# Kernel optimization log

Measured on AMD Instinct MI355X. Metric: run time of the kernel, lower is better.

Reference implementation:

```python
import jax, jax.numpy as jnp
import numpy as np

DIM_H = 128
N_EXPERTS = 4
N_GRAPHS = 256
EPS = 1e-5


def setup_inputs() -> dict:
    key = jax.random.key(0)
    ks = jax.random.split(key, 16)
    N, E, D = 100000, 1600000, DIM_H
    x = jax.random.normal(ks[0], (N, D), dtype=jnp.float32)
    edge_index = jax.random.randint(ks[1], (2, E), 0, N, dtype=jnp.int64)
    batch = jnp.sort(jax.random.randint(ks[2], (N,), 0, N_GRAPHS, dtype=jnp.int64))
    s = 0.05
    gin = 2 * D + 4  # router input: mean | max | 4 graph stats
    params = dict(
        temperature=jnp.ones((1,), jnp.float32) * 2.0,
        rw1=jax.random.normal(ks[3], (gin, D), jnp.float32) * s,
        rb1=jnp.zeros((D,), jnp.float32),
        rw2=jax.random.normal(ks[4], (D, D // 2), jnp.float32) * s,
        rb2=jnp.zeros((D // 2,), jnp.float32),
        rw3=jax.random.normal(ks[5], (D // 2, N_EXPERTS), jnp.float32) * s,
        rb3=jnp.zeros((N_EXPERTS,), jnp.float32),
        expert_w=jax.random.normal(ks[6], (N_EXPERTS, D, D), jnp.float32) * s,
        expert_b=jnp.zeros((N_EXPERTS, D), jnp.float32),
        bn1_g=jnp.ones((D,), jnp.float32),
        bn1_b=jnp.zeros((D,), jnp.float32),
        ff_w1=jax.random.normal(ks[7], (D, 2 * D), jnp.float32) * s,
        ff_b1=jnp.zeros((2 * D,), jnp.float32),
        ff_w2=jax.random.normal(ks[8], (2 * D, D), jnp.float32) * s,
        ff_b2=jnp.zeros((D,), jnp.float32),
        bn2_g=jnp.ones((D,), jnp.float32),
        bn2_b=jnp.zeros((D,), jnp.float32),
    )
    return dict(x=x, edge_index=edge_index, batch=batch, **params)


def _gcn_agg(x, src, dst, n):
    deg = jnp.zeros((n,), x.dtype).at[dst].add(1.0) + 1.0
    dinv = jax.lax.rsqrt(deg)
    coef = dinv[src] * dinv[dst]                        # [E]
    agg = jax.ops.segment_sum(x[src] * coef[:, None], dst, num_segments=n)
    return agg + x * (1.0 / deg)[:, None]               # self-loop term (coef = 1/deg)


def _batchnorm(h, g, b):
    mu = jnp.mean(h, axis=0)
    var = jnp.var(h, axis=0)
    return (h - mu) * jax.lax.rsqrt(var + EPS) * g + b


def reference(x, edge_index, batch, temperature, rw1, rb1, rw2, rb2, rw3, rb3,
              expert_w, expert_b, bn1_g, bn1_b, ff_w1, ff_b1, ff_w2, ff_b2,
              bn2_g, bn2_b):
    n = x.shape[0]
    src, dst = edge_index[0], edge_index[1]
    B = N_GRAPHS

    # ---- graph embeddings: [mean_pool | max_pool | 4 stats] -> [B, 2D+4] ----
    cnt = jnp.maximum(jax.ops.segment_sum(jnp.ones((n,), x.dtype), batch, num_segments=B), 1.0)
    gmean = jax.ops.segment_sum(x, batch, num_segments=B) / cnt[:, None]
    gmax = jax.ops.segment_max(x, batch, num_segments=B)
    node_deg = jnp.zeros((n,), x.dtype).at[dst].add(1.0)
    mean_deg = jax.ops.segment_sum(node_deg, batch, num_segments=B) / cnt
    max_deg = jax.ops.segment_max(node_deg, batch, num_segments=B)
    stats = jnp.stack([cnt, mean_deg, max_deg, jnp.log(cnt)], axis=-1)  # [B,4]
    ge = jnp.concatenate([gmean, gmax, stats], axis=-1)

    # ---- router: MLP + temperature softmax -> [B, E] ----
    h = jax.nn.relu(ge @ rw1 + rb1)
    h = jax.nn.relu(h @ rw2 + rb2)
    scores = h @ rw3 + rb3
    gates = jax.nn.softmax(scores / temperature, axis=-1)   # [B, n_experts]

    # ---- experts: GCNConv_i(x). Aggregation is linear so do it once. ----
    agg = _gcn_agg(x, src, dst, n)                          # [N, D]
    expert_out = jnp.einsum('nd,edo->neo', agg, expert_w) + expert_b[None]  # [N,E,D]

    # ---- softmax-gated combine with per-graph gates ----
    kv = jnp.einsum('neo,ne->no', expert_out, gates[batch])  # [N, D]

    # ---- residual + batchnorm + FFN block ----
    kv = _batchnorm(x + kv, bn1_g, bn1_b)
    ff = jax.nn.relu(kv @ ff_w1 + ff_b1) @ ff_w2 + ff_b2
    out = _batchnorm(kv + ff, bn2_g, bn2_b)
    return out
```

## Files before the change

### kernel.cpp

```cpp
#include <hip/hip_runtime.h>
#include <math.h>

#define D 128
#define B 256
#define EPSV 1e-5f
#define NREP 64

typedef __attribute__((ext_vector_type(8))) short short8;
typedef __attribute__((ext_vector_type(4))) float f32x4;

static __device__ __forceinline__ ushort f2bf(float f) {
  union { float f; unsigned u; } v; v.f = f;
  unsigned r = (v.u + 0x7fffu + ((v.u >> 16) & 1u)) >> 16;
  return (ushort)r;
}
static __device__ __forceinline__ float bf2f(ushort u) {
  union { unsigned u; float f; } v; v.u = ((unsigned)u) << 16; return v.f;
}
static __device__ __forceinline__ unsigned encf(float f) {
  union { float f; unsigned u; } v; v.f = f;
  return (v.u & 0x80000000u) ? ~v.u : (v.u | 0x80000000u);
}
static __device__ __forceinline__ float decf(unsigned e) {
  union { unsigned u; float f; } v;
  v.u = (e & 0x80000000u) ? (e & 0x7FFFFFFFu) : ~e;
  return v.f;
}
#define ENC_NEGINF 0x007FFFFFu

static __global__ void init_kernel(int* bcnt, float* bn1s, float* bn1s2,
                                   float* bn2s, float* bn2s2,
                                   float* gsum, unsigned* gmaxE,
                                   float* gcnt, float* gdsum, unsigned* gdmaxE, int N) {
  int i = blockIdx.x * 256 + threadIdx.x;
  if (i < 256) bcnt[i] = 0;
  if (i < NREP * D) { bn1s[i] = 0.f; bn1s2[i] = 0.f; bn2s[i] = 0.f; bn2s2[i] = 0.f; }
  if (i < B * D) { gsum[i] = 0.f; gmaxE[i] = ENC_NEGINF; }
  if (i < B) { gcnt[i] = 0.f; gdsum[i] = 0.f; gdmaxE[i] = ENC_NEGINF; }
}

static __global__ void __launch_bounds__(256) bhist_kernel(
    const int* __restrict__ dst, int* bcnt, int E) {
  __shared__ int histS[256];
  int t = threadIdx.x;
  int base = blockIdx.x * 4096;
  histS[t] = 0;
  __syncthreads();
#pragma unroll
  for (int k = 0; k < 16; k++) {
    int e = base + k * 256 + t;
    if (e < E) atomicAdd(&histS[dst[e] >> 9], 1);
  }
  __syncthreads();
  int hv = histS[t];
  if (hv > 0) atomicAdd(&bcnt[t], hv);
}

static __global__ void bscan_kernel(const int* __restrict__ bcnt, int* bbase, int* bcur) {
  __shared__ int sS[256];
  int t = threadIdx.x;
  int v = bcnt[t];
  sS[t] = v; __syncthreads();
  for (int off = 1; off < 256; off <<= 1) {
    int add = (t >= off) ? sS[t - off] : 0;
    __syncthreads();
    sS[t] += add;
    __syncthreads();
  }
  int incl = sS[t];
  bbase[t + 1] = incl;
  bcur[t] = incl - v;
  if (t == 0) bbase[0] = 0;
}

static __global__ void statspart_kernel(const float* __restrict__ x, const int* __restrict__ batch,
                                        const float* __restrict__ dinv,
                                        float* gsum, unsigned* gmaxE,
                                        ushort* __restrict__ x_bf, int N) {
  __shared__ float dS[64];
  int t = threadIdx.x;
  int n0 = blockIdx.x * 64;
  int nend = min(n0 + 64, N);
  if (t < 64 && n0 + t < N) dS[t] = dinv[n0 + t];
  __syncthreads();
  int curg = batch[n0];
  float s = 0.f, mx = -INFINITY;
  for (int n = n0; n < nend; n++) {
    int g = batch[n];
    if (g != curg) {
      atomicAdd(&gsum[curg * D + t], s);
      atomicMax(&gmaxE[curg * D + t], encf(mx));
      s = 0.f; mx = -INFINITY; curg = g;
    }
    float v = x[(size_t)n * D + t];
    x_bf[(size_t)n * D + t] = f2bf(v * dS[n - n0]);
    s += v; mx = fmaxf(mx, v);
  }
  atomicAdd(&gsum[curg * D + t], s);
  atomicMax(&gmaxE[curg * D + t], encf(mx));
}

static __global__ void router_kernel(
    const float* __restrict__ gsum, const unsigned* __restrict__ gmaxE,
    const float* __restrict__ gcnt, const float* __restrict__ gdsum,
    const unsigned* __restrict__ gdmaxE,
    const float* __restrict__ rw1, const float* __restrict__ rb1,
    const float* __restrict__ rw2, const float* __restrict__ rb2,
    const float* __restrict__ rw3, const float* __restrict__ rb3,
    const float* __restrict__ temp, float* __restrict__ gates) {
  int g = blockIdx.x, t = threadIdx.x;
  __shared__ float geS[260], h1S[D], h2S[64], scS[4];
  float cntf = fmaxf(gcnt[g], 1.f);
  geS[t] = gsum[g * D + t] / cntf;
  geS[D + t] = decf(gmaxE[g * D + t]);
  if (t == 0) {
    geS[256] = cntf;
    geS[257] = gdsum[g] / cntf;
    geS[258] = decf(gdmaxE[g]);
    geS[259] = logf(cntf);
  }
  __syncthreads();
  float a = rb1[t];
  for (int k = 0; k < 260; k++) a += geS[k] * rw1[k * D + t];
  h1S[t] = fmaxf(a, 0.f);
  __syncthreads();
  if (t < 64) { float b = rb2[t]; for (int k = 0; k < D; k++) b += h1S[k] * rw2[k * 64 + t]; h2S[t] = fmaxf(b, 0.f); }
  __syncthreads();
  if (t < 4) { float c = rb3[t]; for (int k = 0; k < 64; k++) c += h2S[k] * rw3[k * 4 + t]; scS[t] = c; }
  __syncthreads();
  if (t == 0) {
    float T = temp[0];
    float q0 = scS[0] / T, q1 = scS[1] / T, q2 = scS[2] / T, q3 = scS[3] / T;
    float m = fmaxf(fmaxf(q0, q1), fmaxf(q2, q3));
    float e0 = expf(q0 - m), e1 = expf(q1 - m), e2 = expf(q2 - m), e3 = expf(q3 - m);
    float inv = 1.f / (e0 + e1 + e2 + e3);
    gates[g * 4 + 0] = e0 * inv; gates[g * 4 + 1] = e1 * inv;
    gates[g * 4 + 2] = e2 * inv; gates[g * 4 + 3] = e3 * inv;
  }
}

static __global__ void __launch_bounds__(256) wcomb_kernel(
    const float* __restrict__ gates, const float* __restrict__ ew,
    const float* __restrict__ eb, ushort* __restrict__ W_combT,
    float* __restrict__ b_comb) {
  __shared__ ushort wS[128 * 130];
  int g = blockIdx.x, t = threadIdx.x;
  float g0 = gates[g * 4], g1 = gates[g * 4 + 1], g2 = gates[g * 4 + 2], g3 = gates[g * 4 + 3];
  for (int k = t; k < D * D; k += 256) {
    int d = k >> 7, o = k & 127;
    float v = g0 * ew[k] + g1 * ew[16384 + k] + g2 * ew[32768 + k] + g3 * ew[49152 + k];
    wS[o * 130 + d] = f2bf(v);
  }
  __syncthreads();
  for (int k = t; k < D * D; k += 256) {
    int o = k >> 7, d = k & 127;
    W_combT[(size_t)g * 16384 + k] = wS[o * 130 + d];
  }
  if (t < D)
    b_comb[g * D + t] = g0 * eb[t] + g1 * eb[D + t] + g2 * eb[2 * D + t] + g3 * eb[3 * D + t];
}

static __global__ void prep_kernel(const float* __restrict__ w1, const float* __restrict__ w2,
                                   ushort* __restrict__ w1t, ushort* __restrict__ w2t) {
  int i = blockIdx.x * 256 + threadIdx.x;
  { int j = i >> 7, d = i & 127; w1t[i] = f2bf(w1[(size_t)d * 256 + j]); }
  { int o = i >> 8, j = i & 255; w2t[i] = f2bf(w2[(size_t)j * 128 + o]); }
}

static __global__ void __launch_bounds__(256) fillA_kernel(
    const int* __restrict__ src, const int* __restrict__ dst,
    int* bcur, int* __restrict__ esort, int E) {
  __shared__ int histS[256], startS[256], cursorS[256], gbaseS[256];
  __shared__ int eS[4096];
  __shared__ unsigned char bS[4096];
  int t = threadIdx.x;
  int base = blockIdx.x * 4096;
  int cnt = min(4096, E - base);
  int srcR[16], dstR[16];
  histS[t] = 0;
  __syncthreads();
#pragma unroll
  for (int k = 0; k < 16; k++) {
    int e = base + k * 256 + t;
    if (e < E) { srcR[k] = src[e]; dstR[k] = dst[e]; }
    else dstR[k] = -1;
  }
#pragma unroll
  for (int k = 0; k < 16; k++)
    if (dstR[k] >= 0) atomicAdd(&histS[dstR[k] >> 9], 1);
  __syncthreads();
  int hv = histS[t];
  startS[t] = hv;
  __syncthreads();
  for (int off = 1; off < 256; off <<= 1) {
    int add = (t >= off) ? startS[t - off] : 0;
    __syncthreads();
    startS[t] += add;
    __syncthreads();
  }
  int excl = startS[t] - hv;
  __syncthreads();
  startS[t] = excl;
  cursorS[t] = excl;
  gbaseS[t] = (hv > 0) ? atomicAdd(&bcur[t], hv) : 0;
  __syncthreads();
#pragma unroll
  for (int k = 0; k < 16; k++)
    if (dstR[k] >= 0) {
      int b = dstR[k] >> 9;
      int p = atomicAdd(&cursorS[b], 1);
      eS[p] = (srcR[k] << 9) | (dstR[k] & 511);
      bS[p] = (unsigned char)b;
    }
  __syncthreads();
  for (int k = t; k < cnt; k += 256) {
    int b = bS[k];
    esort[gbaseS[b] + (k - startS[b])] = eS[k];
  }
}

static __global__ void __launch_bounds__(256) fillB_kernel(
    const int* __restrict__ esort, const int* __restrict__ bbase,
    int* __restrict__ rowoff, int* __restrict__ node_deg, float* __restrict__ dinv,
    int* __restrict__ csr_src, int N) {
  __shared__ int degS[512];
  __shared__ int pS[256];
  __shared__ int curS[512];
  int b = blockIdx.x, t = threadIdx.x;
  int n0 = b << 9, n1 = min(n0 + 512, N);
  int nn = n1 - n0;
  int r0 = bbase[b], r1 = bbase[b + 1];
  degS[t] = 0; degS[t + 256] = 0;
  __syncthreads();
  for (int e = r0 + t; e < r1; e += 256) atomicAdd(&degS[esort[e] & 511], 1);
  __syncthreads();
  int d0 = degS[2 * t], d1 = degS[2 * t + 1];
  int ps = d0 + d1;
  pS[t] = ps;
  __syncthreads();
  for (int off = 1; off < 256; off <<= 1) {
    int add = (t >= off) ? pS[t - off] : 0;
    __syncthreads();
    pS[t] += add;
    __syncthreads();
  }
  int pexcl = pS[t] - ps;
  int e0 = pexcl, e1 = pexcl + d0;
  curS[2 * t] = r0 + e0;
  curS[2 * t + 1] = r0 + e1;
  int i0 = 2 * t, i1 = 2 * t + 1;
  if (i0 < nn) {
    rowoff[n0 + i0 + 1] = r0 + e0 + d0;
    node_deg[n0 + i0] = d0;
    dinv[n0 + i0] = rsqrtf((float)d0 + 1.f);
  }
  if (i1 < nn) {
    rowoff[n0 + i1 + 1] = r0 + e1 + d1;
    node_deg[n0 + i1] = d1;
    dinv[n0 + i1] = rsqrtf((float)d1 + 1.f);
  }
  if (b == 0 && t == 0) rowoff[0] = 0;
  __syncthreads();
  for (int e = r0 + t; e < r1; e += 256) {
    int v = esort[e];
    int p = atomicAdd(&curS[v & 511], 1);
    csr_src[p] = v >> 9;
  }
}

static __global__ void nodestats_kernel(const int* __restrict__ node_deg,
                                        const int* __restrict__ batch,
                                        float* gcnt, float* gdsum, unsigned* gdmaxE, int N) {
  int i = blockIdx.x * 256 + threadIdx.x;
  int nd = (i < N) ? node_deg[i] : 0;
  int g = batch[min(i, N - 1)];
  float dv = (float)nd;
  int g0w = __shfl(g, 0);
  int waveLast = blockIdx.x * 256 + ((threadIdx.x >> 6) << 6) + 63;
  bool uni = (waveLast < N) && __all(g == g0w);
  if (uni) {
    float s = dv, mx = dv;
    for (int off = 32; off > 0; off >>= 1) { s += __shfl_down(s, off); mx = fmaxf(mx, __shfl_down(mx, off)); }
    if ((threadIdx.x & 63) == 0) {
      atomicAdd(&gcnt[g0w], 64.f);
      atomicAdd(&gdsum[g0w], s);
      atomicMax(&gdmaxE[g0w], encf(mx));
    }
  } else if (i < N) {
    atomicAdd(&gcnt[g], 1.f);
    atomicAdd(&gdsum[g], dv);
    atomicMax(&gdmaxE[g], encf(dv));
  }
}

static __global__ void __launch_bounds__(256) gather_kernel(
    const ushort* __restrict__ xb, const int* __restrict__ rowoff,
    const int* __restrict__ csr_src, const float* __restrict__ dinv,
    ushort* __restrict__ aggB, int N) {
  __shared__ int eS[4][64];
  int t = threadIdx.x, w = t >> 6, l = t & 63;
  int n = blockIdx.x * 4 + w;
  if (n >= N) return;
  int h = l >> 4;
  int f8 = (l & 15) * 8;
  int r0 = rowoff[n], r1 = rowoff[n + 1];
  float dn = dinv[n];
  short8 xo = *(const short8*)&xb[(size_t)n * D + f8];
  float acc[8];
#pragma unroll
  for (int i = 0; i < 8; i++) acc[i] = 0.f;
  int pads = 0;
  for (int j0 = r0; j0 < r1; j0 += 64) {
    int cnt = min(64, r1 - j0);
    int cnt4 = (cnt + 3) & ~3;
    pads += cnt4 - cnt;
    eS[w][l] = (j0 + l < r1) ? csr_src[j0 + l] : n;
    int k = 0;
    for (; k + 8 <= cnt4; k += 8) {
      int s0 = eS[w][k + h];
      int s1 = eS[w][k + 4 + h];
      short8 v0 = *(const short8*)&xb[(size_t)s0 * D + f8];
      short8 v1 = *(const short8*)&xb[(size_t)s1 * D + f8];
#pragma unroll
      for (int i = 0; i < 8; i++) acc[i] += bf2f((ushort)v0[i]);
#pragma unroll
      for (int i = 0; i < 8; i++) acc[i] += bf2f((ushort)v1[i]);
    }
    if (k < cnt4) {
      int s0 = eS[w][k + h];
      short8 v0 = *(const short8*)&xb[(size_t)s0 * D + f8];
#pragma unroll
      for (int i = 0; i < 8; i++) acc[i] += bf2f((ushort)v0[i]);
    }
  }
#pragma unroll
  for (int i = 0; i < 8; i++) {
    acc[i] += __shfl_down(acc[i], 32);
    acc[i] += __shfl_down(acc[i], 16);
  }
  if (l < 16) {
    float wn = 1.f - (float)pads;
    short8 o;
#pragma unroll
    for (int i = 0; i < 8; i++) {
      float v = dn * (acc[i] + wn * bf2f((ushort)xo[i]));
      o[i] = (short)f2bf(v);
    }
    *(short8*)&aggB[(size_t)n * D + f8] = o;
  }
}

static __global__ void __launch_bounds__(512, 4) expert_kernel(
    const ushort* __restrict__ aggB, const float* __restrict__ x, const int* __restrict__ batch,
    const ushort* __restrict__ W_combT, const float* __restrict__ b_comb,
    ushort* __restrict__ hB, float* bn1s, float* bn1s2, int N) {
  __shared__ __align__(16) ushort aggS[64 * 136];
  __shared__ int bS[64];
  int t = threadIdx.x, n0 = blockIdx.x * 64;
  int tile = min(64, N - n0);
  for (int k = t; k < 64 * 16; k += 512) {
    int i = k >> 4, c = (k & 15) * 8;
    short8 v = (short8){0, 0, 0, 0, 0, 0, 0, 0};
    if (i < tile) v = *(const short8*)&aggB[(size_t)(n0 + i) * D + c];
    *(short8*)&aggS[i * 136 + c] = v;
  }
  if (t < 64) bS[t] = batch[min(n0 + t, N - 1)];
  __syncthreads();
  int w = t >> 6, ln = t & 15, quad = (t & 63) >> 4;
  int o = w * 16 + ln;
  float s = 0.f, s2 = 0.f;
  int mstart = 0;
  while (mstart < tile) {
    int g = bS[mstart];
    int mend = mstart + 1;
    while (mend < tile && bS[mend] == g) mend++;
    f32x4 acc[4];
#pragma unroll
    for (int mi = 0; mi < 4; mi++) acc[mi] = (f32x4){0.f, 0.f, 0.f, 0.f};
    const ushort* Wg = W_combT + (size_t)g * 16384;
#pragma unroll
    for (int ks = 0; ks < 4; ks++) {
      int kk = ks * 32 + quad * 8;
      short8 a[4], b;
#pragma unroll
      for (int mi = 0; mi < 4; mi++) a[mi] = *(const short8*)&aggS[(mi * 16 + ln) * 136 + kk];
      b = *(const short8*)&Wg[(size_t)o * 128 + kk];
#pragma unroll
      for (int mi = 0; mi < 4; mi++)
        acc[mi] = __builtin_amdgcn_mfma_f32_16x16x32_bf16(a[mi], b, acc[mi], 0, 0, 0);
    }
    float bias = b_comb[g * D + o];
#pragma unroll
    for (int mi = 0; mi < 4; mi++)
#pragma unroll
      for (int r = 0; r < 4; r++) {
        int m = mi * 16 + quad * 4 + r;
        if (m >= mstart && m < mend) {
          size_t ro = (size_t)(n0 + m) * D;
          float hv = x[ro + o] + acc[mi][r] + bias;
          hB[ro + o] = f2bf(hv);
          s += hv; s2 += hv * hv;
        }
      }
    mstart = mend;
  }
  s += __shfl_down(s, 32);  s += __shfl_down(s, 16);
  s2 += __shfl_down(s2, 32); s2 += __shfl_down(s2, 16);
  if (quad == 0) {
    int slot = (blockIdx.x & (NREP - 1)) * D;
    atomicAdd(&bn1s[slot + o], s);
    atomicAdd(&bn1s2[slot + o], s2);
  }
}

static __global__ void bnfin_kernel(const float* s, const float* s2,
                                    const float* __restrict__ g, const float* __restrict__ b,
                                    float* sc, float* sh, float invN) {
  int t = threadIdx.x;
  if (t < D) {
    float st = 0.f, s2t = 0.f;
    for (int k = 0; k < NREP; k++) { st += s[k * D + t]; s2t += s2[k * D + t]; }
    float m = st * invN;
    float var = s2t * invN - m * m;
    float rstd = rsqrtf(var + EPSV);
    float scv = rstd * g[t];
    sc[t] = scv;
    sh[t] = b[t] - m * scv;
  }
}

static __global__ void __launch_bounds__(512, 4) ffn_kernel(
    ushort* __restrict__ hB, const float* __restrict__ sc1, const float* __restrict__ sh1,
    const ushort* __restrict__ w1t, const float* __restrict__ fb1,
    const ushort* __restrict__ w2t, const float* __restrict__ fb2,
    float* bn2s, float* bn2s2, int N) {
  __shared__ __align__(16) ushort kvnS[64 * 136];
  __shared__ __align__(16) ushort hidS[64 * 264];
  int t = threadIdx.x, n0 = blockIdx.x * 64;
  int tile = min(64, N - n0);
  for (int k = t; k < 64 * 64; k += 512) {
    int i = k >> 6, dp = (k & 63) * 2;
    float vx = 0.f, vy = 0.f;
    if (i < tile) {
      ushort2 hv = *(const ushort2*)&hB[(size_t)(n0 + i) * D + dp];
      vx = bf2f(hv.x) * sc1[dp] + sh1[dp];
      vy = bf2f(hv.y) * sc1[dp + 1] + sh1[dp + 1];
    }
    kvnS[i * 136 + dp] = f2bf(vx);
    kvnS[i * 136 + dp + 1] = f2bf(vy);
  }
  __syncthreads();
  int w = t >> 6, ln = t & 15, quad = (t & 63) >> 4;
  f32x4 acc1[4][2];
#pragma unroll
  for (int mi = 0; mi < 4; mi++)
#pragma unroll
    for (int ni = 0; ni < 2; ni++) acc1[mi][ni] = (f32x4){0.f, 0.f, 0.f, 0.f};
#pragma unroll
  for (int ks = 0; ks < 4; ks++) {
    int kk = ks * 32 + quad * 8;
    short8 a[4], b[2];
#pragma unroll
    for (int mi = 0; mi < 4; mi++) a[mi] = *(const short8*)&kvnS[(mi * 16 + ln) * 136 + kk];
#pragma unroll
    for (int ni = 0; ni < 2; ni++) b[ni] = *(const short8*)&w1t[(size_t)(w * 32 + ni * 16 + ln) * 128 + kk];
#pragma unroll
    for (int mi = 0; mi < 4; mi++)
#pragma unroll
      for (int ni = 0; ni < 2; ni++)
        acc1[mi][ni] = __builtin_amdgcn_mfma_f32_16x16x32_bf16(a[mi], b[ni], acc1[mi][ni], 0, 0, 0);
  }
  float bias1[2];
#pragma unroll
  for (int ni = 0; ni < 2; ni++) bias1[ni] = fb1[w * 32 + ni * 16 + ln];
#pragma unroll
  for (int mi = 0; mi < 4; mi++)
#pragma unroll
    for (int ni = 0; ni < 2; ni++)
#pragma unroll
      for (int r = 0; r < 4; r++) {
        int mrow = mi * 16 + quad * 4 + r;
        int j = w * 32 + ni * 16 + ln;
        hidS[mrow * 264 + j] = f2bf(fmaxf(acc1[mi][ni][r] + bias1[ni], 0.f));
      }
  __syncthreads();
  int o = w * 16 + ln;
  f32x4 acc2[4];
#pragma unroll
  for (int mi = 0; mi < 4; mi++) acc2[mi] = (f32x4){0.f, 0.f, 0.f, 0.f};
#pragma unroll
  for (int ks = 0; ks < 8; ks++) {
    int kk = ks * 32 + quad * 8;
    short8 a[4], b;
#pragma unroll
    for (int mi = 0; mi < 4; mi++) a[mi] = *(const short8*)&hidS[(mi * 16 + ln) * 264 + kk];
    b = *(const short8*)&w2t[(size_t)o * 256 + kk];
#pragma unroll
    for (int mi = 0; mi < 4; mi++)
      acc2[mi] = __builtin_amdgcn_mfma_f32_16x16x32_bf16(a[mi], b, acc2[mi], 0, 0, 0);
  }
  float bias2 = fb2[o];
  float s = 0.f, s2 = 0.f;
#pragma unroll
  for (int mi = 0; mi < 4; mi++)
#pragma unroll
    for (int r = 0; r < 4; r++) {
      int mrow = mi * 16 + quad * 4 + r;
      if (mrow < tile) {
        size_t ro = (size_t)(n0 + mrow) * D;
        float v = bf2f(kvnS[mrow * 136 + o]) + acc2[mi][r] + bias2;
        hB[ro + o] = f2bf(v);
        s += v; s2 += v * v;
      }
    }
  s += __shfl_down(s, 32);  s += __shfl_down(s, 16);
  s2 += __shfl_down(s2, 32); s2 += __shfl_down(s2, 16);
  if (quad == 0) {
    int slot = (blockIdx.x & (NREP - 1)) * D;
    atomicAdd(&bn2s[slot + o], s);
    atomicAdd(&bn2s2[slot + o], s2);
  }
}

static __global__ void bnapply_kernel(const ushort* __restrict__ hB, float* __restrict__ out,
                                      const float* __restrict__ sc, const float* __restrict__ sh,
                                      int total) {
  int i = blockIdx.x * 256 + threadIdx.x;
  if (i < total) {
    int d = i & 127;
    out[i] = bf2f(hB[i]) * sc[d] + sh[d];
  }
}

extern "C" void kernel_launch(void* const* d_in, const int* in_sizes, int n_in,
                              void* d_out, int out_size, void* d_ws, size_t ws_size,
                              hipStream_t stream) {
  (void)n_in; (void)out_size; (void)ws_size;
  const float* x    = (const float*)d_in[0];
  const int*   ei   = (const int*)d_in[1];
  const int*   batch= (const int*)d_in[2];
  const float* temp = (const float*)d_in[3];
  const float* rw1  = (const float*)d_in[4];
  const float* rb1  = (const float*)d_in[5];
  const float* rw2  = (const float*)d_in[6];
  const float* rb2  = (const float*)d_in[7];
  const float* rw3  = (const float*)d_in[8];
  const float* rb3  = (const float*)d_in[9];
  const float* ew   = (const float*)d_in[10];
  const float* eb   = (const float*)d_in[11];
  const float* bn1g = (const float*)d_in[12];
  const float* bn1b = (const float*)d_in[13];
  const float* fw1  = (const float*)d_in[14];
  const float* fb1  = (const float*)d_in[15];
  const float* fw2  = (const float*)d_in[16];
  const float* fb2  = (const float*)d_in[17];
  const float* bn2g = (const float*)d_in[18];
  const float* bn2b = (const float*)d_in[19];

  int N = in_sizes[0] / D;
  int E = in_sizes[1] / 2;
  const int* src = ei;
  const int* dst = ei + E;

  ushort* x_bf = (ushort*)d_out;
  ushort* aggB = (ushort*)((char*)d_out + (size_t)N * D * 2);

  char* p = (char*)d_ws;
  auto alloc = [&](size_t bytes) -> void* {
    void* r = (void*)p;
    p += (bytes + 255) & ~(size_t)255;
    return r;
  };
  int NB = (N + 511) >> 9;
  int*   node_deg = (int*)alloc((size_t)N * 4);
  int*   rowoff   = (int*)alloc(((size_t)N + 1) * 4);
  int*   csr_src  = (int*)alloc((size_t)E * 4);
  int*   esort    = (int*)alloc((size_t)E * 4);
  int*   bcnt     = (int*)alloc(256 * 4);
  int*   bbase    = (int*)alloc(257 * 4);
  int*   bcur     = (int*)alloc(256 * 4);
  float* dinv     = (float*)alloc((size_t)N * 4);
  ushort* hB      = (ushort*)alloc((size_t)N * D * 2);
  float* gsum     = (float*)alloc((size_t)B * D * 4);
  unsigned* gmaxE = (unsigned*)alloc((size_t)B * D * 4);
  float* gcnt     = (float*)alloc((size_t)B * 4);
  float* gdsum    = (float*)alloc((size_t)B * 4);
  unsigned* gdmaxE= (unsigned*)alloc((size_t)B * 4);
  float* gates    = (float*)alloc((size_t)B * 4 * 4);
  float* b_comb   = (float*)alloc((size_t)B * D * 4);
  float* bn1s     = (float*)alloc((size_t)NREP * D * 4);
  float* bn1s2    = (float*)alloc((size_t)NREP * D * 4);
  float* sc1      = (float*)alloc(D * 4);
  float* sh1      = (float*)alloc(D * 4);
  float* bn2s     = (float*)alloc((size_t)NREP * D * 4);
  float* bn2s2    = (float*)alloc((size_t)NREP * D * 4);
  float* sc2      = (float*)alloc(D * 4);
  float* sh2      = (float*)alloc(D * 4);
  ushort* W_combT = (ushort*)alloc((size_t)B * D * D * 2);
  ushort* w1t     = (ushort*)alloc((size_t)D * 256 * 2);
  ushort* w2t     = (ushort*)alloc((size_t)D * 256 * 2);

  init_kernel<<<(N + 255) / 256, 256, 0, stream>>>(bcnt, bn1s, bn1s2, bn2s, bn2s2,
                                                   gsum, gmaxE, gcnt, gdsum, gdmaxE, N);
  prep_kernel<<<128, 256, 0, stream>>>(fw1, fw2, w1t, w2t);
  bhist_kernel<<<(E + 4095) / 4096, 256, 0, stream>>>(dst, bcnt, E);
  bscan_kernel<<<1, 256, 0, stream>>>(bcnt, bbase, bcur);
  fillA_kernel<<<(E + 4095) / 4096, 256, 0, stream>>>(src, dst, bcur, esort, E);
  fillB_kernel<<<NB, 256, 0, stream>>>(esort, bbase, rowoff, node_deg, dinv, csr_src, N);
  nodestats_kernel<<<(N + 255) / 256, 256, 0, stream>>>(node_deg, batch, gcnt, gdsum, gdmaxE, N);
  statspart_kernel<<<(N + 63) / 64, 128, 0, stream>>>(x, batch, dinv, gsum, gmaxE, x_bf, N);
  router_kernel<<<B, 128, 0, stream>>>(gsum, gmaxE, gcnt, gdsum, gdmaxE,
                                       rw1, rb1, rw2, rb2, rw3, rb3, temp, gates);
  wcomb_kernel<<<B, 256, 0, stream>>>(gates, ew, eb, W_combT, b_comb);
  gather_kernel<<<(N + 3) / 4, 256, 0, stream>>>(x_bf, rowoff, csr_src, dinv, aggB, N);
  int nb64 = (N + 63) / 64;
  expert_kernel<<<nb64, 512, 0, stream>>>(aggB, x, batch, W_combT, b_comb, hB, bn1s, bn1s2, N);
  bnfin_kernel<<<1, 128, 0, stream>>>(bn1s, bn1s2, bn1g, bn1b, sc1, sh1, 1.0f / (float)N);
  ffn_kernel<<<nb64, 512, 0, stream>>>(hB, sc1, sh1, w1t, fb1, w2t, fb2, bn2s, bn2s2, N);
  bnfin_kernel<<<1, 128, 0, stream>>>(bn2s, bn2s2, bn2g, bn2b, sc2, sh2, 1.0f / (float)N);
  bnapply_kernel<<<((size_t)N * D + 255) / 256, 256, 0, stream>>>(hB, (float*)d_out, sc2, sh2, N * D);
}
```

Baseline: 510.9 us.

## Halve expert block size, widen per-wave N tile, and remap tiles per XCD

The expert GEMM kernel now runs with 256 threads per block, and each wave computes two 16-column output tiles instead of one. This reuses the A fragments read from LDS across two MFMAs and halves the LDS A traffic per output. Block indices are also remapped so that each XCD handles a contiguous range of node tiles, which aims to keep the per-graph combined weights in that XCD's L2. The cost is more accumulator registers per wave and fewer waves per block to hide latency.

```diff
diff --git a/kernel.cpp b/kernel.cpp
--- a/kernel.cpp
+++ b/kernel.cpp
@@ -350,15 +350,20 @@
   }
 }
 
-static __global__ void __launch_bounds__(512, 4) expert_kernel(
+static __global__ void __launch_bounds__(256) expert_kernel(
     const ushort* __restrict__ aggB, const float* __restrict__ x, const int* __restrict__ batch,
     const ushort* __restrict__ W_combT, const float* __restrict__ b_comb,
     ushort* __restrict__ hB, float* bn1s, float* bn1s2, int N) {
   __shared__ __align__(16) ushort aggS[64 * 136];
   __shared__ int bS[64];
-  int t = threadIdx.x, n0 = blockIdx.x * 64;
+  int t = threadIdx.x;
+  int nwg = gridDim.x;
+  int q = nwg >> 3, r = nwg & 7;
+  int xcd = blockIdx.x & 7, ix = blockIdx.x >> 3;
+  int tilei = (xcd < r) ? (xcd * (q + 1) + ix) : (r * (q + 1) + (xcd - r) * q + ix);
+  int n0 = tilei * 64;
   int tile = min(64, N - n0);
-  for (int k = t; k < 64 * 16; k += 512) {
+  for (int k = t; k < 64 * 16; k += 256) {
     int i = k >> 4, c = (k & 15) * 8;
     short8 v = (short8){0, 0, 0, 0, 0, 0, 0, 0};
     if (i < tile) v = *(const short8*)&aggB[(size_t)(n0 + i) * D + c];
@@ -367,49 +372,66 @@
   if (t < 64) bS[t] = batch[min(n0 + t, N - 1)];
   __syncthreads();
   int w = t >> 6, ln = t & 15, quad = (t & 63) >> 4;
-  int o = w * 16 + ln;
-  float s = 0.f, s2 = 0.f;
+  float s[2] = {0.f, 0.f}, s2[2] = {0.f, 0.f};
   int mstart = 0;
   while (mstart < tile) {
     int g = bS[mstart];
     int mend = mstart + 1;
     while (mend < tile && bS[mend] == g) mend++;
-    f32x4 acc[4];
-#pragma unroll
-    for (int mi = 0; mi < 4; mi++) acc[mi] = (f32x4){0.f, 0.f, 0.f, 0.f};
+    f32x4 acc[4][2];
+#pragma unroll
+    for (int mi = 0; mi < 4; mi++)
+#pragma unroll
+      for (int ni = 0; ni < 2; ni++) acc[mi][ni] = (f32x4){0.f, 0.f, 0.f, 0.f};
     const ushort* Wg = W_combT + (size_t)g * 16384;
 #pragma unroll
     for (int ks = 0; ks < 4; ks++) {
       int kk = ks * 32 + quad * 8;
-      short8 a[4], b;
+      short8 a[4], b[2];
 #pragma unroll
       for (int mi = 0; mi < 4; mi++) a[mi] = *(const short8*)&aggS[(mi * 16 + ln) * 136 + kk];
-      b = *(const short8*)&Wg[(size_t)o * 128 + kk];
+#pragma unroll
+      for (int ni = 0; ni < 2; ni++) b[ni] = *(const short8*)&Wg[(size_t)(w * 32 + ni * 16 + ln) * 128 + kk];
 #pragma unroll
       for (int mi = 0; mi < 4; mi++)
-        acc[mi] = __builtin_amdgcn_mfma_f32_16x16x32_bf16(a[mi], b, acc[mi], 0, 0, 0);
-    }
-    float bias = b_comb[g * D + o];
+#pragma unroll
+        for (int ni = 0; ni < 2; ni++)
+          acc[mi][ni] = __builtin_amdgcn_mfma_f32_16x16x32_bf16(a[mi], b[ni], acc[mi][ni], 0, 0, 0);
+    }
+    float bias[2];
+#pragma unroll
+    for (int ni = 0; ni < 2; ni++) bias[ni] = b_comb[g * D + w * 32 + ni * 16 + ln];
 #pragma unroll
     for (int mi = 0; mi < 4; mi++)
 #pragma unroll
-      for (int r = 0; r < 4; r++) {
-        int m = mi * 16 + quad * 4 + r;
+      for (int r2_ = 0; r2_ < 4; r2_++) {
+        int m = mi * 16 + quad * 4 + r2_;
         if (m >= mstart && m < mend) {
-          size_t ro = (size_t)(n0 + m) * D;
-          float hv = x[ro + o] + acc[mi][r] + bias;
-          hB[ro + o] = f2bf(hv);
-          s += hv; s2 += hv * hv;
+          size_t rowoff_ = (size_t)(n0 + m) * D;
+#pragma unroll
+          for (int ni = 0; ni < 2; ni++) {
+            int o = w * 32 + ni * 16 + ln;
+            float hv = x[rowoff_ + o] + acc[mi][ni][r2_] + bias[ni];
+            hB[rowoff_ + o] = f2bf(hv);
+            s[ni] += hv; s2[ni] += hv * hv;
+          }
         }
       }
     mstart = mend;
   }
-  s += __shfl_down(s, 32);  s += __shfl_down(s, 16);
-  s2 += __shfl_down(s2, 32); s2 += __shfl_down(s2, 16);
+#pragma unroll
+  for (int ni = 0; ni < 2; ni++) {
+    s[ni] += __shfl_down(s[ni], 32);  s[ni] += __shfl_down(s[ni], 16);
+    s2[ni] += __shfl_down(s2[ni], 32); s2[ni] += __shfl_down(s2[ni], 16);
+  }
   if (quad == 0) {
-    int slot = (blockIdx.x & (NREP - 1)) * D;
-    atomicAdd(&bn1s[slot + o], s);
-    atomicAdd(&bn1s2[slot + o], s2);
+    int slot = (tilei & (NREP - 1)) * D;
+#pragma unroll
+    for (int ni = 0; ni < 2; ni++) {
+      int o = w * 32 + ni * 16 + ln;
+      atomicAdd(&bn1s[slot + o], s[ni]);
+      atomicAdd(&bn1s2[slot + o], s2[ni]);
+    }
   }
 }
 
@@ -614,7 +636,7 @@
   wcomb_kernel<<<B, 256, 0, stream>>>(gates, ew, eb, W_combT, b_comb);
   gather_kernel<<<(N + 3) / 4, 256, 0, stream>>>(x_bf, rowoff, csr_src, dinv, aggB, N);
   int nb64 = (N + 63) / 64;
-  expert_kernel<<<nb64, 512, 0, stream>>>(aggB, x, batch, W_combT, b_comb, hB, bn1s, bn1s2, N);
+  expert_kernel<<<nb64, 256, 0, stream>>>(aggB, x, batch, W_combT, b_comb, hB, bn1s, bn1s2, N);
   bnfin_kernel<<<1, 128, 0, stream>>>(bn1s, bn1s2, bn1g, bn1b, sc1, sh1, 1.0f / (float)N);
   ffn_kernel<<<nb64, 512, 0, stream>>>(hB, sc1, sh1, w1t, fb1, w2t, fb2, bn2s, bn2s2, N);
   bnfin_kernel<<<1, 128, 0, stream>>>(bn2s, bn2s2, bn2g, bn2b, sc2, sh2, 1.0f / (float)N);
```

New measurement: 477.4 us. 1.07x faster.
